# Kernel tuning notes

Hardware: AMD Instinct MI355X
Metric: run time of the kernel (lower is better)

The kernel has to match this reference:

```python
import jax, jax.numpy as jnp
import numpy as np

N, E, D, L = 50000, 640000, 128, 3  # nodes, edges, channels, layers
EPS = 1e-5


def setup_inputs() -> dict:
    key = jax.random.key(0)
    ks = jax.random.split(key, 10)
    s = 1.0 / np.sqrt(D)
    inp = {
        "x": jax.random.normal(ks[0], (N, D), dtype=jnp.float32),
        "edge_attr": jax.random.normal(ks[1], (E, D), dtype=jnp.float32),
        "w_self": jax.random.normal(ks[2], (L, D, D), dtype=jnp.float32) * s,
        "b_self": jnp.zeros((L, D), dtype=jnp.float32),
        "w_in": jax.random.normal(ks[3], (L, D, D), dtype=jnp.float32) * s,
        "b_in": jnp.zeros((L, D), dtype=jnp.float32),
        "w_rel": jax.random.normal(ks[4], (L, D, D), dtype=jnp.float32) * s,
        "b_rel": jnp.zeros((L, D), dtype=jnp.float32),
        "bn_gamma": jnp.ones((L - 1, D), dtype=jnp.float32),
        "bn_beta": jnp.zeros((L - 1, D), dtype=jnp.float32),
        "edge_index": jax.random.randint(ks[5], (2, E), 0, N, dtype=jnp.int64),
    }
    return inp


def _batchnorm(h, gamma, beta):
    mu = jnp.mean(h, axis=0)
    var = jnp.mean(jnp.square(h - mu), axis=0)  # biased var (torch BN training)
    return (h - mu) * jax.lax.rsqrt(var + EPS) * gamma + beta


def reference(x, edge_attr, w_self, b_self, w_in, b_in, w_rel, b_rel,
              bn_gamma, bn_beta, edge_index):
    src, dst = edge_index[0], edge_index[1]
    # per-node in-degree for mean aggregation (zero-degree nodes -> 0)
    cnt = jax.ops.segment_sum(jnp.ones((E, 1), x.dtype), dst, num_segments=N)
    denom = jnp.maximum(cnt, 1.0)
    for i in range(L):
        # message: lin_in(x_j * edge_attr)
        msg = jnp.einsum('ed,fd->ef', x[src] * edge_attr, w_in[i]) + b_in[i]
        agg = jax.ops.segment_sum(msg, dst, num_segments=N) / denom  # scatter-mean
        x = agg + jnp.einsum('nd,fd->nf', x, w_self[i]) + b_self[i]
        edge_attr = jnp.einsum('ed,fd->ef', edge_attr, w_rel[i]) + b_rel[i]
        if i < L - 1:
            x = jax.nn.relu(_batchnorm(x, bn_gamma[i], bn_beta[i]))
            # dropout p=0.0 -> identity
    return (x, edge_attr)
```

## Files before the change

### kernel.cpp

```cpp
#include <hip/hip_runtime.h>

#define DD 128

typedef __attribute__((ext_vector_type(8))) short bf16x8;
typedef __attribute__((ext_vector_type(4))) short bf16x4;
typedef __attribute__((ext_vector_type(4))) float f32x4;
typedef unsigned short u16;

__device__ __forceinline__ unsigned short f2bf(float f) {
  union { float f; unsigned u; } v; v.f = f;
  unsigned u = v.u;
  return (unsigned short)((u + 0x7FFFu + ((u >> 16) & 1u)) >> 16);
}
__device__ __forceinline__ float bf2f(unsigned short h) {
  union { unsigned u; float f; } v; v.u = ((unsigned)h) << 16; return v.f;
}
__device__ __forceinline__ bf16x8 pack8(f32x4 a, f32x4 b) {
  bf16x8 r;
  r[0] = (short)f2bf(a.x); r[1] = (short)f2bf(a.y);
  r[2] = (short)f2bf(a.z); r[3] = (short)f2bf(a.w);
  r[4] = (short)f2bf(b.x); r[5] = (short)f2bf(b.y);
  r[6] = (short)f2bf(b.z); r[7] = (short)f2bf(b.w);
  return r;
}

__device__ __forceinline__ bool idx_is64(const int* p) {
  return (p[1] | p[3] | p[5] | p[7]) == 0;
}
__device__ __forceinline__ int ld_idx(const int* p, long long i, bool is64) {
  return is64 ? (int)((const long long*)p)[i] : p[i];
}

__global__ void k_count(const int* __restrict__ idx, int* __restrict__ cnt, int E) {
  int e = blockIdx.x * blockDim.x + threadIdx.x;
  if (e >= E) return;
  bool is64 = idx_is64(idx);
  int d = ld_idx(idx, (long long)E + e, is64);
  atomicAdd(&cnt[d], 1);
}

__global__ __launch_bounds__(1024) void k_scan(const int* __restrict__ cnt,
    int* __restrict__ row_start, int* __restrict__ cursor, int N) {
  __shared__ int part[1024];
  int t = threadIdx.x;
  int chunk = (N + 1023) >> 10;
  int lo = t * chunk, hi = lo + chunk; if (hi > N) hi = N; if (lo > N) lo = N;
  int s = 0;
  for (int i = lo; i < hi; ++i) s += cnt[i];
  part[t] = s;
  __syncthreads();
  for (int off = 1; off < 1024; off <<= 1) {
    int v = (t >= off) ? part[t - off] : 0;
    __syncthreads();
    part[t] += v;
    __syncthreads();
  }
  int run = (t == 0) ? 0 : part[t - 1];
  for (int i = lo; i < hi; ++i) {
    row_start[i] = run; cursor[i] = run; run += cnt[i];
  }
  if (t == 1023) row_start[N] = part[1023];
}

__global__ void k_fill(const int* __restrict__ idx, int* __restrict__ cursor,
                       int* __restrict__ edge_of, int* __restrict__ src_csr,
                       int* __restrict__ inv, int E) {
  int e = blockIdx.x * blockDim.x + threadIdx.x;
  if (e >= E) return;
  bool is64 = idx_is64(idx);
  int s = ld_idx(idx, e, is64);
  int d = ld_idx(idx, (long long)E + e, is64);
  int pos = atomicAdd(&cursor[d], 1);
  edge_of[pos] = e;
  src_csr[pos] = s;
  inv[e] = pos;
}

template <int MODE>
__global__ __launch_bounds__(256) void k_layer(
    const float* __restrict__ x0, const u16* __restrict__ xbin,
    const float* __restrict__ ea0, const u16* __restrict__ eain,
    u16* __restrict__ xbout, float* __restrict__ xfout,
    u16* __restrict__ eabout, float* __restrict__ eafout,
    const int* __restrict__ row_start, const int* __restrict__ edge_of,
    const int* __restrict__ src_csr, const int* __restrict__ inv,
    const float* __restrict__ w_in, const float* __restrict__ w_self,
    const float* __restrict__ b_in, const float* __restrict__ b_self,
    const float* __restrict__ w_rel, const float* __restrict__ b_rel,
    const float* __restrict__ scale, const float* __restrict__ shift,
    float* __restrict__ gsum, float* __restrict__ gssq,
    int ntN, int ntE, int strideB) {
  __shared__ short LDS[40960];
  int bid = blockIdx.x;
  int tid = threadIdx.x;
  int wave = tid >> 6, lane = tid & 63;
  bool isA = (bid % 5) == 4;

  if (isA) {
    for (int q = tid; q < 8192; q += 256) {
      int off = q * 4;
      int f = off >> 8, k = off & 255;
      f32x4 w = (k < 128) ? *(const f32x4*)(w_in + f * 128 + k)
                          : *(const f32x4*)(w_self + f * 128 + (k - 128));
      unsigned byte = ((unsigned)(f * 512 + k * 2)) ^ (unsigned)((f & 7) << 4);
      bf16x4 s4;
      s4[0] = (short)f2bf(w.x); s4[1] = (short)f2bf(w.y);
      s4[2] = (short)f2bf(w.z); s4[3] = (short)f2bf(w.w);
      *(bf16x4*)((char*)LDS + byte) = s4;
    }
    __syncthreads();
    int tile = (bid / 5) * 4 + wave;
    if (tile >= ntN) return;
    short* aggL = LDS + 32768 + wave * 2048;
    int esub = lane >> 4, cg = lane & 15;
    int c0g = cg * 8;
    float scA[8], shA[8];
    if constexpr (MODE >= 1) {
#pragma unroll
      for (int j = 0; j < 8; ++j) { scA[j] = scale[c0g + j]; shA[j] = shift[c0g + j]; }
    }
    for (int n16 = 0; n16 < 16; ++n16) {
      int n = tile * 16 + n16;
      int s0 = row_start[n], s1 = row_start[n + 1];
      int len = s1 - s0;
      float acc[8];
#pragma unroll
      for (int j = 0; j < 8; ++j) acc[j] = 0.f;
      for (int kk = 0; kk < len; kk += 4) {
        int kx = kk + esub;
        bool act = kx < len;
        int k = s0 + (act ? kx : 0);
        if constexpr (MODE == 0) {
          int e = edge_of[k];
          int sn = src_csr[k];
          const float* ep = ea0 + (size_t)e * DD + c0g;
          f32x4 e0 = *(const f32x4*)ep, e1 = *(const f32x4*)(ep + 4);
          const float* xp = x0 + (size_t)sn * DD + c0g;
          f32x4 xv0 = *(const f32x4*)xp, xv1 = *(const f32x4*)(xp + 4);
          if (act) {
#pragma unroll
            for (int j = 0; j < 4; ++j) { acc[j] += xv0[j] * e0[j]; acc[4 + j] += xv1[j] * e1[j]; }
          }
        } else {
          int sn = src_csr[k];
          bf16x8 ev = *(const bf16x8*)(eain + (size_t)k * DD + c0g);
          bf16x8 xv = *(const bf16x8*)(xbin + (size_t)sn * DD + c0g);
          if (act) {
#pragma unroll
            for (int j = 0; j < 8; ++j) {
              float xf = fmaxf(bf2f((u16)xv[j]) * scA[j] + shA[j], 0.f);
              acc[j] += xf * bf2f((u16)ev[j]);
            }
          }
        }
      }
      float invd = (len > 0) ? 1.0f / (float)len : 0.0f;
#pragma unroll
      for (int j = 0; j < 8; ++j) {
        float s = acc[j];
        s += __shfl_xor(s, 16);
        s += __shfl_xor(s, 32);
        acc[j] = s * invd;
      }
      if (esub == 0) {
        f32x4 lo, hi;
#pragma unroll
        for (int j = 0; j < 4; ++j) { lo[j] = acc[j]; hi[j] = acc[4 + j]; }
        *(bf16x8*)(aggL + n16 * 128 + ((cg ^ (n16 & 15)) * 8)) = pack8(lo, hi);
      }
    }
    asm volatile("s_waitcnt lgkmcnt(0)" ::: "memory");
    int r = lane & 15, g = lane >> 4;
    bf16x8 a8[8];
#pragma unroll
    for (int ks = 0; ks < 4; ++ks)
      a8[ks] = *(const bf16x8*)(aggL + r * 128 + (((ks * 4 + g) ^ (r & 15)) * 8));
#pragma unroll
    for (int ks = 0; ks < 4; ++ks) {
      int c0 = ks * 32 + g * 8;
      if constexpr (MODE == 0) {
        const float* p = x0 + (size_t)(tile * 16 + r) * DD + c0;
        a8[4 + ks] = pack8(*(const f32x4*)p, *(const f32x4*)(p + 4));
      } else {
        bf16x8 raw = *(const bf16x8*)(xbin + (size_t)(tile * 16 + r) * DD + c0);
        bf16x8 fr;
#pragma unroll
        for (int j = 0; j < 8; ++j) {
          float f = fmaxf(bf2f((u16)raw[j]) * scale[c0 + j] + shift[c0 + j], 0.f);
          fr[j] = (short)f2bf(f);
        }
        a8[4 + ks] = fr;
      }
    }
    f32x4 acc4[8];
#pragma unroll
    for (int ct = 0; ct < 8; ++ct) acc4[ct] = (f32x4){0.f, 0.f, 0.f, 0.f};
#pragma unroll
    for (int ct = 0; ct < 8; ++ct) {
      int f = ct * 16 + r;
      unsigned base = (unsigned)(f * 512);
      unsigned sw = (unsigned)((f & 7) << 4);
#pragma unroll
      for (int ks = 0; ks < 8; ++ks) {
        unsigned byte = (base + (unsigned)(ks * 64 + g * 16)) ^ sw;
        bf16x8 b = *(const bf16x8*)((const char*)LDS + byte);
        acc4[ct] = __builtin_amdgcn_mfma_f32_16x16x32_bf16(a8[ks], b, acc4[ct], 0, 0, 0);
      }
    }
    int nbase = tile * 16;
    float degmask[4];
#pragma unroll
    for (int j = 0; j < 4; ++j) {
      int nn = nbase + g * 4 + j;
      degmask[j] = (row_start[nn + 1] > row_start[nn]) ? 1.0f : 0.0f;
    }
#pragma unroll
    for (int ct = 0; ct < 8; ++ct) {
      int col = ct * 16 + r;
      float bi = b_in[col], bs = b_self[col];
      float s = 0.f, s2 = 0.f;
#pragma unroll
      for (int j = 0; j < 4; ++j) {
        float v = acc4[ct][j] + bs + bi * degmask[j];
        if constexpr (MODE < 2) xbout[(size_t)(nbase + g * 4 + j) * DD + col] = f2bf(v);
        else                    xfout[(size_t)(nbase + g * 4 + j) * DD + col] = v;
        s += v; s2 += v * v;
      }
      if constexpr (MODE < 2) {
        s += __shfl_xor(s, 16);  s += __shfl_xor(s, 32);
        s2 += __shfl_xor(s2, 16); s2 += __shfl_xor(s2, 32);
        if (g == 0) { atomicAdd(&gsum[col], s); atomicAdd(&gssq[col], s2); }
      }
    }
  } else {
    int b = bid - (bid + 1) / 5;
    for (int q = tid; q < 4096; q += 256) {
      int off = q * 4;
      int f = off >> 7, d = off & 127;
      f32x4 w = *(const f32x4*)(w_rel + off);
      unsigned byte = ((unsigned)(f * 256 + d * 2)) ^ (unsigned)((f & 7) << 4);
      bf16x4 s4;
      s4[0] = (short)f2bf(w.x); s4[1] = (short)f2bf(w.y);
      s4[2] = (short)f2bf(w.z); s4[3] = (short)f2bf(w.w);
      *(bf16x4*)((char*)LDS + byte) = s4;
    }
    __syncthreads();
    int r = lane & 15, g = lane >> 4;
    for (int tile = b * 4 + wave; tile < ntE; tile += strideB) {
      bf16x8 a8[4];
      if constexpr (MODE == 0) {
        const float* rp = ea0 + (size_t)(tile * 16 + r) * DD;
#pragma unroll
        for (int ks = 0; ks < 4; ++ks) {
          const float* p = rp + ks * 32 + g * 8;
          a8[ks] = pack8(*(const f32x4*)p, *(const f32x4*)(p + 4));
        }
      } else {
        const u16* rp = eain + (size_t)(tile * 16 + r) * DD;
#pragma unroll
        for (int ks = 0; ks < 4; ++ks) a8[ks] = *(const bf16x8*)(rp + ks * 32 + g * 8);
      }
      f32x4 acc4[8];
#pragma unroll
      for (int ct = 0; ct < 8; ++ct) acc4[ct] = (f32x4){0.f, 0.f, 0.f, 0.f};
#pragma unroll
      for (int ct = 0; ct < 8; ++ct) {
        int f = ct * 16 + r;
        unsigned base = (unsigned)(f * 256);
        unsigned sw = (unsigned)((f & 7) << 4);
#pragma unroll
        for (int ks = 0; ks < 4; ++ks) {
          unsigned byte = (base + (unsigned)(ks * 64 + g * 16)) ^ sw;
          bf16x8 bb = *(const bf16x8*)((const char*)LDS + byte);
          acc4[ct] = __builtin_amdgcn_mfma_f32_16x16x32_bf16(a8[ks], bb, acc4[ct], 0, 0, 0);
        }
      }
      size_t orow[4];
#pragma unroll
      for (int j = 0; j < 4; ++j) {
        int kr = tile * 16 + g * 4 + j;
        if constexpr (MODE == 0)      orow[j] = (size_t)inv[kr];
        else if constexpr (MODE == 1) orow[j] = (size_t)kr;
        else                          orow[j] = (size_t)edge_of[kr];
      }
#pragma unroll
      for (int ct = 0; ct < 8; ++ct) {
        int col = ct * 16 + r;
        float bv = b_rel[col];
#pragma unroll
        for (int j = 0; j < 4; ++j) {
          float v = acc4[ct][j] + bv;
          if constexpr (MODE == 2) eafout[orow[j] * DD + col] = v;
          else                     eabout[orow[j] * DD + col] = f2bf(v);
        }
      }
    }
  }
}

__global__ void k_bnfin(float* __restrict__ gsum, float* __restrict__ gssq,
    const float* __restrict__ gamma, const float* __restrict__ beta,
    float* __restrict__ scale, float* __restrict__ shift, int N) {
  int d = threadIdx.x;
  float mu = gsum[d] / (float)N;
  float var = gssq[d] / (float)N - mu * mu;
  float rs = rsqrtf(var + 1e-5f);
  float sc = rs * gamma[d];
  scale[d] = sc;
  shift[d] = beta[d] - mu * sc;
  gsum[d] = 0.f;
  gssq[d] = 0.f;
}

static inline size_t alignup(size_t v, size_t a) { return (v + a - 1) & ~(a - 1); }

extern "C" void kernel_launch(void* const* d_in, const int* in_sizes, int n_in,
                              void* d_out, int out_size, void* d_ws, size_t ws_size,
                              hipStream_t stream) {
  const float* x0     = (const float*)d_in[0];
  const float* ea0    = (const float*)d_in[1];
  const float* w_self = (const float*)d_in[2];
  const float* b_self = (const float*)d_in[3];
  const float* w_in   = (const float*)d_in[4];
  const float* b_in   = (const float*)d_in[5];
  const float* w_rel  = (const float*)d_in[6];
  const float* b_rel  = (const float*)d_in[7];
  const float* gamma  = (const float*)d_in[8];
  const float* beta   = (const float*)d_in[9];
  const int*   idx    = (const int*)d_in[10];

  const int N = in_sizes[0] / DD;
  const int E = in_sizes[1] / DD;

  char* w = (char*)d_ws;
  size_t off = 0;
  int* cnt       = (int*)(w + off); off = alignup(off + (size_t)N * 4, 256);
  int* row_start = (int*)(w + off); off = alignup(off + (size_t)(N + 1) * 4, 256);
  int* cursor    = (int*)(w + off); off = alignup(off + (size_t)N * 4, 256);
  int* edge_of   = (int*)(w + off); off = alignup(off + (size_t)E * 4, 256);
  int* src_csr   = (int*)(w + off); off = alignup(off + (size_t)E * 4, 256);
  int* inv       = (int*)(w + off); off = alignup(off + (size_t)E * 4, 256);
  float* gstats  = (float*)(w + off); off = alignup(off + 256 * 4, 256);
  float* scale   = (float*)(w + off); off = alignup(off + 128 * 4, 256);
  float* shift   = (float*)(w + off); off = alignup(off + 128 * 4, 256);
  u16* xbA       = (u16*)(w + off); off = alignup(off + (size_t)N * DD * 2, 256);
  u16* xbB       = (u16*)(w + off); off = alignup(off + (size_t)N * DD * 2, 256);
  u16* eaA       = (u16*)(w + off); off = alignup(off + (size_t)E * DD * 2, 256);
  u16* eaB       = (u16*)(w + off); off = alignup(off + (size_t)E * DD * 2, 256);
  float* gsum = gstats, *gssq = gstats + 128;
  (void)ws_size; (void)n_in; (void)out_size;

  float* out_x  = (float*)d_out;
  float* out_ea = out_x + (size_t)N * DD;

  (void)hipMemsetAsync(cnt, 0, (size_t)N * 4, stream);
  int ethreads = 256, eblocks = (E + ethreads - 1) / ethreads;
  k_count<<<eblocks, ethreads, 0, stream>>>(idx, cnt, E);
  k_scan<<<1, 1024, 0, stream>>>(cnt, row_start, cursor, N);
  k_fill<<<eblocks, ethreads, 0, stream>>>(idx, cursor, edge_of, src_csr, inv, E);
  (void)hipMemsetAsync(gstats, 0, 256 * 4, stream);

  const int ntN = N / 16;
  const int ntE = E / 16;
  const int nA = (ntN + 3) / 4;
  const int grid = nA * 5;
  const int strideB = (grid - nA) * 4;

  k_layer<0><<<grid, 256, 0, stream>>>(x0, nullptr, ea0, nullptr,
      xbA, nullptr, eaA, nullptr,
      row_start, edge_of, src_csr, inv,
      w_in, w_self, b_in, b_self, w_rel, b_rel,
      scale, shift, gsum, gssq, ntN, ntE, strideB);
  k_bnfin<<<1, 128, 0, stream>>>(gsum, gssq, gamma, beta, scale, shift, N);

  k_layer<1><<<grid, 256, 0, stream>>>(nullptr, xbA, nullptr, eaA,
      xbB, nullptr, eaB, nullptr,
      row_start, edge_of, src_csr, inv,
      w_in + DD * DD, w_self + DD * DD, b_in + DD, b_self + DD,
      w_rel + DD * DD, b_rel + DD,
      scale, shift, gsum, gssq, ntN, ntE, strideB);
  k_bnfin<<<1, 128, 0, stream>>>(gsum, gssq, gamma + DD, beta + DD, scale, shift, N);

  k_layer<2><<<grid, 256, 0, stream>>>(nullptr, xbB, nullptr, eaB,
      nullptr, out_x, nullptr, out_ea,
      row_start, edge_of, src_csr, inv,
      w_in + 2 * DD * DD, w_self + 2 * DD * DD, b_in + 2 * DD, b_self + 2 * DD,
      w_rel + 2 * DD * DD, b_rel + 2 * DD,
      scale, shift, gsum, gssq, ntN, ntE, strideB);
}
```

Before: 1.103 ms.

## Split fused layer kernel into per-node aggregation/edge-GEMM and separate node GEMM

Result: faster. 1.029 ms (-6.8%).

```diff
diff --git a/kernel.cpp b/kernel.cpp
--- a/kernel.cpp
+++ b/kernel.cpp
@@ -63,8 +63,7 @@
 }
 
 __global__ void k_fill(const int* __restrict__ idx, int* __restrict__ cursor,
-                       int* __restrict__ edge_of, int* __restrict__ src_csr,
-                       int* __restrict__ inv, int E) {
+                       int* __restrict__ edge_of, int* __restrict__ src_csr, int E) {
   int e = blockIdx.x * blockDim.x + threadIdx.x;
   if (e >= E) return;
   bool is64 = idx_is64(idx);
@@ -73,167 +72,100 @@
   int pos = atomicAdd(&cursor[d], 1);
   edge_of[pos] = e;
   src_csr[pos] = s;
-  inv[e] = pos;
 }
 
 template <int MODE>
-__global__ __launch_bounds__(256) void k_layer(
+__global__ __launch_bounds__(256, 4) void k_ar(
     const float* __restrict__ x0, const u16* __restrict__ xbin,
     const float* __restrict__ ea0, const u16* __restrict__ eain,
-    u16* __restrict__ xbout, float* __restrict__ xfout,
     u16* __restrict__ eabout, float* __restrict__ eafout,
+    float* __restrict__ aggmf, u16* __restrict__ aggm,
     const int* __restrict__ row_start, const int* __restrict__ edge_of,
-    const int* __restrict__ src_csr, const int* __restrict__ inv,
-    const float* __restrict__ w_in, const float* __restrict__ w_self,
-    const float* __restrict__ b_in, const float* __restrict__ b_self,
+    const int* __restrict__ src_csr,
     const float* __restrict__ w_rel, const float* __restrict__ b_rel,
     const float* __restrict__ scale, const float* __restrict__ shift,
-    float* __restrict__ gsum, float* __restrict__ gssq,
-    int ntN, int ntE, int strideB) {
-  __shared__ short LDS[40960];
+    int nA, int ntE) {
+  __shared__ short Wl[16384];
   int bid = blockIdx.x;
   int tid = threadIdx.x;
   int wave = tid >> 6, lane = tid & 63;
-  bool isA = (bid % 5) == 4;
-
-  if (isA) {
-    for (int q = tid; q < 8192; q += 256) {
-      int off = q * 4;
-      int f = off >> 8, k = off & 255;
-      f32x4 w = (k < 128) ? *(const f32x4*)(w_in + f * 128 + k)
-                          : *(const f32x4*)(w_self + f * 128 + (k - 128));
-      unsigned byte = ((unsigned)(f * 512 + k * 2)) ^ (unsigned)((f & 7) << 4);
-      bf16x4 s4;
-      s4[0] = (short)f2bf(w.x); s4[1] = (short)f2bf(w.y);
-      s4[2] = (short)f2bf(w.z); s4[3] = (short)f2bf(w.w);
-      *(bf16x4*)((char*)LDS + byte) = s4;
-    }
-    __syncthreads();
-    int tile = (bid / 5) * 4 + wave;
-    if (tile >= ntN) return;
-    short* aggL = LDS + 32768 + wave * 2048;
+  (void)aggmf;
+
+  if (bid < nA) {
+    int n = bid * 4 + wave;
     int esub = lane >> 4, cg = lane & 15;
-    int c0g = cg * 8;
+    int c0 = cg * 8;
     float scA[8], shA[8];
     if constexpr (MODE >= 1) {
 #pragma unroll
-      for (int j = 0; j < 8; ++j) { scA[j] = scale[c0g + j]; shA[j] = shift[c0g + j]; }
-    }
-    for (int n16 = 0; n16 < 16; ++n16) {
-      int n = tile * 16 + n16;
-      int s0 = row_start[n], s1 = row_start[n + 1];
-      int len = s1 - s0;
-      float acc[8];
-#pragma unroll
-      for (int j = 0; j < 8; ++j) acc[j] = 0.f;
-      for (int kk = 0; kk < len; kk += 4) {
-        int kx = kk + esub;
-        bool act = kx < len;
-        int k = s0 + (act ? kx : 0);
-        if constexpr (MODE == 0) {
-          int e = edge_of[k];
-          int sn = src_csr[k];
-          const float* ep = ea0 + (size_t)e * DD + c0g;
-          f32x4 e0 = *(const f32x4*)ep, e1 = *(const f32x4*)(ep + 4);
-          const float* xp = x0 + (size_t)sn * DD + c0g;
-          f32x4 xv0 = *(const f32x4*)xp, xv1 = *(const f32x4*)(xp + 4);
-          if (act) {
-#pragma unroll
-            for (int j = 0; j < 4; ++j) { acc[j] += xv0[j] * e0[j]; acc[4 + j] += xv1[j] * e1[j]; }
+      for (int j = 0; j < 8; ++j) { scA[j] = scale[c0 + j]; shA[j] = shift[c0 + j]; }
+    }
+    int s0 = row_start[n], s1 = row_start[n + 1];
+    int len = s1 - s0;
+    float acc[8];
+#pragma unroll
+    for (int j = 0; j < 8; ++j) acc[j] = 0.f;
+    for (int kk = 0; kk < len; kk += 8) {
+      int kx0 = kk + esub, kx1 = kk + 4 + esub;
+      bool a0 = kx0 < len, a1 = kx1 < len;
+      int k0 = s0 + (a0 ? kx0 : 0);
+      int k1 = s0 + (a1 ? kx1 : 0);
+      if constexpr (MODE == 0) {
+        int e0 = edge_of[k0], e1 = edge_of[k1];
+        int sn0 = src_csr[k0], sn1 = src_csr[k1];
+        const float* ep0 = ea0 + (size_t)e0 * DD + c0;
+        const float* ep1 = ea0 + (size_t)e1 * DD + c0;
+        const float* xp0 = x0 + (size_t)sn0 * DD + c0;
+        const float* xp1 = x0 + (size_t)sn1 * DD + c0;
+        f32x4 ea0a = *(const f32x4*)ep0, ea0b = *(const f32x4*)(ep0 + 4);
+        f32x4 ea1a = *(const f32x4*)ep1, ea1b = *(const f32x4*)(ep1 + 4);
+        f32x4 xv0a = *(const f32x4*)xp0, xv0b = *(const f32x4*)(xp0 + 4);
+        f32x4 xv1a = *(const f32x4*)xp1, xv1b = *(const f32x4*)(xp1 + 4);
+        if (a0) {
+#pragma unroll
+          for (int j = 0; j < 4; ++j) { acc[j] += xv0a[j] * ea0a[j]; acc[4 + j] += xv0b[j] * ea0b[j]; }
+        }
+        if (a1) {
+#pragma unroll
+          for (int j = 0; j < 4; ++j) { acc[j] += xv1a[j] * ea1a[j]; acc[4 + j] += xv1b[j] * ea1b[j]; }
+        }
+      } else {
+        int sn0 = src_csr[k0], sn1 = src_csr[k1];
+        bf16x8 ev0 = *(const bf16x8*)(eain + (size_t)k0 * DD + c0);
+        bf16x8 ev1 = *(const bf16x8*)(eain + (size_t)k1 * DD + c0);
+        bf16x8 xv0 = *(const bf16x8*)(xbin + (size_t)sn0 * DD + c0);
+        bf16x8 xv1 = *(const bf16x8*)(xbin + (size_t)sn1 * DD + c0);
+        if (a0) {
+#pragma unroll
+          for (int j = 0; j < 8; ++j) {
+            float xf = fmaxf(bf2f((u16)xv0[j]) * scA[j] + shA[j], 0.f);
+            acc[j] += xf * bf2f((u16)ev0[j]);
           }
-        } else {
-          int sn = src_csr[k];
-          bf16x8 ev = *(const bf16x8*)(eain + (size_t)k * DD + c0g);
-          bf16x8 xv = *(const bf16x8*)(xbin + (size_t)sn * DD + c0g);
-          if (act) {
-#pragma unroll
-            for (int j = 0; j < 8; ++j) {
-              float xf = fmaxf(bf2f((u16)xv[j]) * scA[j] + shA[j], 0.f);
-              acc[j] += xf * bf2f((u16)ev[j]);
-            }
+        }
+        if (a1) {
+#pragma unroll
+          for (int j = 0; j < 8; ++j) {
+            float xf = fmaxf(bf2f((u16)xv1[j]) * scA[j] + shA[j], 0.f);
+            acc[j] += xf * bf2f((u16)ev1[j]);
           }
         }
       }
-      float invd = (len > 0) ? 1.0f / (float)len : 0.0f;
-#pragma unroll
-      for (int j = 0; j < 8; ++j) {
-        float s = acc[j];
-        s += __shfl_xor(s, 16);
-        s += __shfl_xor(s, 32);
-        acc[j] = s * invd;
-      }
-      if (esub == 0) {
-        f32x4 lo, hi;
-#pragma unroll
-        for (int j = 0; j < 4; ++j) { lo[j] = acc[j]; hi[j] = acc[4 + j]; }
-        *(bf16x8*)(aggL + n16 * 128 + ((cg ^ (n16 & 15)) * 8)) = pack8(lo, hi);
-      }
-    }
-    asm volatile("s_waitcnt lgkmcnt(0)" ::: "memory");
-    int r = lane & 15, g = lane >> 4;
-    bf16x8 a8[8];
-#pragma unroll
-    for (int ks = 0; ks < 4; ++ks)
-      a8[ks] = *(const bf16x8*)(aggL + r * 128 + (((ks * 4 + g) ^ (r & 15)) * 8));
-#pragma unroll
-    for (int ks = 0; ks < 4; ++ks) {
-      int c0 = ks * 32 + g * 8;
-      if constexpr (MODE == 0) {
-        const float* p = x0 + (size_t)(tile * 16 + r) * DD + c0;
-        a8[4 + ks] = pack8(*(const f32x4*)p, *(const f32x4*)(p + 4));
-      } else {
-        bf16x8 raw = *(const bf16x8*)(xbin + (size_t)(tile * 16 + r) * DD + c0);
-        bf16x8 fr;
-#pragma unroll
-        for (int j = 0; j < 8; ++j) {
-          float f = fmaxf(bf2f((u16)raw[j]) * scale[c0 + j] + shift[c0 + j], 0.f);
-          fr[j] = (short)f2bf(f);
-        }
-        a8[4 + ks] = fr;
-      }
-    }
-    f32x4 acc4[8];
-#pragma unroll
-    for (int ct = 0; ct < 8; ++ct) acc4[ct] = (f32x4){0.f, 0.f, 0.f, 0.f};
-#pragma unroll
-    for (int ct = 0; ct < 8; ++ct) {
-      int f = ct * 16 + r;
-      unsigned base = (unsigned)(f * 512);
-      unsigned sw = (unsigned)((f & 7) << 4);
-#pragma unroll
-      for (int ks = 0; ks < 8; ++ks) {
-        unsigned byte = (base + (unsigned)(ks * 64 + g * 16)) ^ sw;
-        bf16x8 b = *(const bf16x8*)((const char*)LDS + byte);
-        acc4[ct] = __builtin_amdgcn_mfma_f32_16x16x32_bf16(a8[ks], b, acc4[ct], 0, 0, 0);
-      }
-    }
-    int nbase = tile * 16;
-    float degmask[4];
-#pragma unroll
-    for (int j = 0; j < 4; ++j) {
-      int nn = nbase + g * 4 + j;
-      degmask[j] = (row_start[nn + 1] > row_start[nn]) ? 1.0f : 0.0f;
-    }
-#pragma unroll
-    for (int ct = 0; ct < 8; ++ct) {
-      int col = ct * 16 + r;
-      float bi = b_in[col], bs = b_self[col];
-      float s = 0.f, s2 = 0.f;
-#pragma unroll
-      for (int j = 0; j < 4; ++j) {
-        float v = acc4[ct][j] + bs + bi * degmask[j];
-        if constexpr (MODE < 2) xbout[(size_t)(nbase + g * 4 + j) * DD + col] = f2bf(v);
-        else                    xfout[(size_t)(nbase + g * 4 + j) * DD + col] = v;
-        s += v; s2 += v * v;
-      }
-      if constexpr (MODE < 2) {
-        s += __shfl_xor(s, 16);  s += __shfl_xor(s, 32);
-        s2 += __shfl_xor(s2, 16); s2 += __shfl_xor(s2, 32);
-        if (g == 0) { atomicAdd(&gsum[col], s); atomicAdd(&gssq[col], s2); }
-      }
+    }
+    float invd = (len > 0) ? 1.0f / (float)len : 0.0f;
+#pragma unroll
+    for (int j = 0; j < 8; ++j) {
+      float s = acc[j];
+      s += __shfl_xor(s, 16);
+      s += __shfl_xor(s, 32);
+      acc[j] = s * invd;
+    }
+    if (esub == 0) {
+      f32x4 lo, hi;
+#pragma unroll
+      for (int j = 0; j < 4; ++j) { lo[j] = acc[j]; hi[j] = acc[4 + j]; }
+      *(bf16x8*)(aggm + (size_t)n * DD + c0) = pack8(lo, hi);
     }
   } else {
-    int b = bid - (bid + 1) / 5;
     for (int q = tid; q < 4096; q += 256) {
       int off = q * 4;
       int f = off >> 7, d = off & 127;
@@ -242,58 +174,149 @@
       bf16x4 s4;
       s4[0] = (short)f2bf(w.x); s4[1] = (short)f2bf(w.y);
       s4[2] = (short)f2bf(w.z); s4[3] = (short)f2bf(w.w);
-      *(bf16x4*)((char*)LDS + byte) = s4;
+      *(bf16x4*)((char*)Wl + byte) = s4;
     }
     __syncthreads();
     int r = lane & 15, g = lane >> 4;
-    for (int tile = b * 4 + wave; tile < ntE; tile += strideB) {
-      bf16x8 a8[4];
-      if constexpr (MODE == 0) {
-        const float* rp = ea0 + (size_t)(tile * 16 + r) * DD;
-#pragma unroll
-        for (int ks = 0; ks < 4; ++ks) {
-          const float* p = rp + ks * 32 + g * 8;
-          a8[ks] = pack8(*(const f32x4*)p, *(const f32x4*)(p + 4));
-        }
-      } else {
-        const u16* rp = eain + (size_t)(tile * 16 + r) * DD;
-#pragma unroll
-        for (int ks = 0; ks < 4; ++ks) a8[ks] = *(const bf16x8*)(rp + ks * 32 + g * 8);
+    int tile = (bid - nA) * 4 + wave;
+    if (tile >= ntE) return;
+    bf16x8 a8[4];
+    if constexpr (MODE == 0) {
+      int er = edge_of[tile * 16 + r];
+      const float* rp = ea0 + (size_t)er * DD;
+#pragma unroll
+      for (int ks = 0; ks < 4; ++ks) {
+        const float* p = rp + ks * 32 + g * 8;
+        a8[ks] = pack8(*(const f32x4*)p, *(const f32x4*)(p + 4));
       }
-      f32x4 acc4[8];
-#pragma unroll
-      for (int ct = 0; ct < 8; ++ct) acc4[ct] = (f32x4){0.f, 0.f, 0.f, 0.f};
-#pragma unroll
-      for (int ct = 0; ct < 8; ++ct) {
-        int f = ct * 16 + r;
-        unsigned base = (unsigned)(f * 256);
-        unsigned sw = (unsigned)((f & 7) << 4);
-#pragma unroll
-        for (int ks = 0; ks < 4; ++ks) {
-          unsigned byte = (base + (unsigned)(ks * 64 + g * 16)) ^ sw;
-          bf16x8 bb = *(const bf16x8*)((const char*)LDS + byte);
-          acc4[ct] = __builtin_amdgcn_mfma_f32_16x16x32_bf16(a8[ks], bb, acc4[ct], 0, 0, 0);
-        }
+    } else {
+      const u16* rp = eain + (size_t)(tile * 16 + r) * DD;
+#pragma unroll
+      for (int ks = 0; ks < 4; ++ks) a8[ks] = *(const bf16x8*)(rp + ks * 32 + g * 8);
+    }
+    f32x4 acc4[8];
+#pragma unroll
+    for (int ct = 0; ct < 8; ++ct) acc4[ct] = (f32x4){0.f, 0.f, 0.f, 0.f};
+#pragma unroll
+    for (int ct = 0; ct < 8; ++ct) {
+      int f = ct * 16 + r;
+      unsigned base = (unsigned)(f * 256);
+      unsigned sw = (unsigned)((f & 7) << 4);
+#pragma unroll
+      for (int ks = 0; ks < 4; ++ks) {
+        unsigned byte = (base + (unsigned)(ks * 64 + g * 16)) ^ sw;
+        bf16x8 bb = *(const bf16x8*)((const char*)Wl + byte);
+        acc4[ct] = __builtin_amdgcn_mfma_f32_16x16x32_bf16(a8[ks], bb, acc4[ct], 0, 0, 0);
       }
-      size_t orow[4];
+    }
+    size_t orow[4];
+#pragma unroll
+    for (int j = 0; j < 4; ++j) {
+      int kr = tile * 16 + g * 4 + j;
+      if constexpr (MODE == 2) orow[j] = (size_t)edge_of[kr];
+      else                     orow[j] = (size_t)kr;
+    }
+#pragma unroll
+    for (int ct = 0; ct < 8; ++ct) {
+      int col = ct * 16 + r;
+      float bv = b_rel[col];
 #pragma unroll
       for (int j = 0; j < 4; ++j) {
-        int kr = tile * 16 + g * 4 + j;
-        if constexpr (MODE == 0)      orow[j] = (size_t)inv[kr];
-        else if constexpr (MODE == 1) orow[j] = (size_t)kr;
-        else                          orow[j] = (size_t)edge_of[kr];
+        float v = acc4[ct][j] + bv;
+        if constexpr (MODE == 2) eafout[orow[j] * DD + col] = v;
+        else                     eabout[orow[j] * DD + col] = f2bf(v);
       }
-#pragma unroll
-      for (int ct = 0; ct < 8; ++ct) {
-        int col = ct * 16 + r;
-        float bv = b_rel[col];
-#pragma unroll
-        for (int j = 0; j < 4; ++j) {
-          float v = acc4[ct][j] + bv;
-          if constexpr (MODE == 2) eafout[orow[j] * DD + col] = v;
-          else                     eabout[orow[j] * DD + col] = f2bf(v);
-        }
+    }
+  }
+}
+
+template <typename TX, bool BN, typename TO, bool STATS>
+__global__ __launch_bounds__(256, 2) void k_node(const u16* __restrict__ aggm,
+    const TX* __restrict__ xc, const float* __restrict__ W_in,
+    const float* __restrict__ W_self, const float* __restrict__ b_in,
+    const float* __restrict__ b_self, const int* __restrict__ row_start,
+    const float* __restrict__ scale, const float* __restrict__ shift,
+    TO* __restrict__ xn, float* __restrict__ gsum, float* __restrict__ gssq,
+    int ntiles) {
+  __shared__ short Wl[DD * 256];
+  for (int q = threadIdx.x; q < DD * 256 / 4; q += 256) {
+    int off = q * 4;
+    int f = off >> 8, k = off & 255;
+    f32x4 w = (k < 128) ? *(const f32x4*)(W_in + f * 128 + k)
+                        : *(const f32x4*)(W_self + f * 128 + (k - 128));
+    unsigned byte = ((unsigned)(f * 512 + k * 2)) ^ (unsigned)((f & 7) << 4);
+    bf16x4 s4;
+    s4[0] = (short)f2bf(w.x); s4[1] = (short)f2bf(w.y);
+    s4[2] = (short)f2bf(w.z); s4[3] = (short)f2bf(w.w);
+    *(bf16x4*)((char*)Wl + byte) = s4;
+  }
+  __syncthreads();
+  int wave = threadIdx.x >> 6, lane = threadIdx.x & 63;
+  int tile = blockIdx.x * 4 + wave;
+  if (tile >= ntiles) return;
+  int r = lane & 15, g = lane >> 4;
+  int arowi = tile * 16 + r;
+  const u16* arow = aggm + (size_t)arowi * DD;
+  const TX* xrow = xc + (size_t)arowi * DD;
+  bf16x8 a[8];
+#pragma unroll
+  for (int ks = 0; ks < 4; ++ks) a[ks] = *(const bf16x8*)(arow + ks * 32 + g * 8);
+#pragma unroll
+  for (int ks = 0; ks < 4; ++ks) {
+    int c0 = ks * 32 + g * 8;
+    if constexpr (sizeof(TX) == 2) {
+      bf16x8 raw = *(const bf16x8*)(xrow + c0);
+      bf16x8 fr;
+#pragma unroll
+      for (int j = 0; j < 8; ++j) {
+        float f = bf2f((u16)raw[j]);
+        if constexpr (BN) f = fmaxf(f * scale[c0 + j] + shift[c0 + j], 0.f);
+        fr[j] = (short)f2bf(f);
       }
+      a[4 + ks] = fr;
+    } else {
+      const float* p = (const float*)xrow + c0;
+      a[4 + ks] = pack8(*(const f32x4*)p, *(const f32x4*)(p + 4));
+    }
+  }
+  f32x4 acc[8];
+#pragma unroll
+  for (int ct = 0; ct < 8; ++ct) acc[ct] = (f32x4){0.f, 0.f, 0.f, 0.f};
+#pragma unroll
+  for (int ct = 0; ct < 8; ++ct) {
+    int f = ct * 16 + r;
+    unsigned base = (unsigned)(f * 512);
+    unsigned sw = (unsigned)((f & 7) << 4);
+#pragma unroll
+    for (int ks = 0; ks < 8; ++ks) {
+      unsigned byte = (base + (unsigned)(ks * 64 + g * 16)) ^ sw;
+      bf16x8 b = *(const bf16x8*)((const char*)Wl + byte);
+      acc[ct] = __builtin_amdgcn_mfma_f32_16x16x32_bf16(a[ks], b, acc[ct], 0, 0, 0);
+    }
+  }
+  int nbase = tile * 16;
+  float degmask[4];
+#pragma unroll
+  for (int j = 0; j < 4; ++j) {
+    int nn = nbase + g * 4 + j;
+    degmask[j] = (row_start[nn + 1] > row_start[nn]) ? 1.0f : 0.0f;
+  }
+#pragma unroll
+  for (int ct = 0; ct < 8; ++ct) {
+    int col = ct * 16 + r;
+    float bi = b_in[col], bs = b_self[col];
+    float s = 0.f, s2 = 0.f;
+#pragma unroll
+    for (int j = 0; j < 4; ++j) {
+      float v = acc[ct][j] + bs + bi * degmask[j];
+      if constexpr (sizeof(TO) == 2) xn[(size_t)(nbase + g * 4 + j) * DD + col] = (TO)f2bf(v);
+      else                            xn[(size_t)(nbase + g * 4 + j) * DD + col] = (TO)v;
+      s += v; s2 += v * v;
+    }
+    if constexpr (STATS) {
+      s += __shfl_xor(s, 16);  s += __shfl_xor(s, 32);
+      s2 += __shfl_xor(s2, 16); s2 += __shfl_xor(s2, 32);
+      if (g == 0) { atomicAdd(&gsum[col], s); atomicAdd(&gssq[col], s2); }
     }
   }
 }
@@ -339,10 +362,10 @@
   int* cursor    = (int*)(w + off); off = alignup(off + (size_t)N * 4, 256);
   int* edge_of   = (int*)(w + off); off = alignup(off + (size_t)E * 4, 256);
   int* src_csr   = (int*)(w + off); off = alignup(off + (size_t)E * 4, 256);
-  int* inv       = (int*)(w + off); off = alignup(off + (size_t)E * 4, 256);
   float* gstats  = (float*)(w + off); off = alignup(off + 256 * 4, 256);
   float* scale   = (float*)(w + off); off = alignup(off + 128 * 4, 256);
   float* shift   = (float*)(w + off); off = alignup(off + 128 * 4, 256);
+  u16* aggm      = (u16*)(w + off); off = alignup(off + (size_t)N * DD * 2, 256);
   u16* xbA       = (u16*)(w + off); off = alignup(off + (size_t)N * DD * 2, 256);
   u16* xbB       = (u16*)(w + off); off = alignup(off + (size_t)N * DD * 2, 256);
   u16* eaA       = (u16*)(w + off); off = alignup(off + (size_t)E * DD * 2, 256);
@@ -357,34 +380,36 @@
   int ethreads = 256, eblocks = (E + ethreads - 1) / ethreads;
   k_count<<<eblocks, ethreads, 0, stream>>>(idx, cnt, E);
   k_scan<<<1, 1024, 0, stream>>>(cnt, row_start, cursor, N);
-  k_fill<<<eblocks, ethreads, 0, stream>>>(idx, cursor, edge_of, src_csr, inv, E);
+  k_fill<<<eblocks, ethreads, 0, stream>>>(idx, cursor, edge_of, src_csr, E);
   (void)hipMemsetAsync(gstats, 0, 256 * 4, stream);
 
   const int ntN = N / 16;
   const int ntE = E / 16;
-  const int nA = (ntN + 3) / 4;
-  const int grid = nA * 5;
-  const int strideB = (grid - nA) * 4;
-
-  k_layer<0><<<grid, 256, 0, stream>>>(x0, nullptr, ea0, nullptr,
-      xbA, nullptr, eaA, nullptr,
-      row_start, edge_of, src_csr, inv,
-      w_in, w_self, b_in, b_self, w_rel, b_rel,
-      scale, shift, gsum, gssq, ntN, ntE, strideB);
+  const int nA = (N + 3) / 4;
+  const int nB = (ntE + 3) / 4;
+  const int grid = nA + nB;
+  const int nodeBlocks = (ntN + 3) / 4;
+
+  k_ar<0><<<grid, 256, 0, stream>>>(x0, nullptr, ea0, nullptr,
+      eaA, nullptr, nullptr, aggm, row_start, edge_of, src_csr,
+      w_rel, b_rel, scale, shift, nA, ntE);
+  k_node<float, false, u16, true><<<nodeBlocks, 256, 0, stream>>>(aggm, x0,
+      w_in, w_self, b_in, b_self, row_start, scale, shift,
+      xbA, gsum, gssq, ntN);
   k_bnfin<<<1, 128, 0, stream>>>(gsum, gssq, gamma, beta, scale, shift, N);
 
-  k_layer<1><<<grid, 256, 0, stream>>>(nullptr, xbA, nullptr, eaA,
-      xbB, nullptr, eaB, nullptr,
-      row_start, edge_of, src_csr, inv,
+  k_ar<1><<<grid, 256, 0, stream>>>(nullptr, xbA, nullptr, eaA,
+      eaB, nullptr, nullptr, aggm, row_start, edge_of, src_csr,
+      w_rel + DD * DD, b_rel + DD, scale, shift, nA, ntE);
+  k_node<u16, true, u16, true><<<nodeBlocks, 256, 0, stream>>>(aggm, xbA,
       w_in + DD * DD, w_self + DD * DD, b_in + DD, b_self + DD,
-      w_rel + DD * DD, b_rel + DD,
-      scale, shift, gsum, gssq, ntN, ntE, strideB);
+      row_start, scale, shift, xbB, gsum, gssq, ntN);
   k_bnfin<<<1, 128, 0, stream>>>(gsum, gssq, gamma + DD, beta + DD, scale, shift, N);
 
-  k_layer<2><<<grid, 256, 0, stream>>>(nullptr, xbB, nullptr, eaB,
-      nullptr, out_x, nullptr, out_ea,
-      row_start, edge_of, src_csr, inv,
+  k_ar<2><<<grid, 256, 0, stream>>>(nullptr, xbB, nullptr, eaB,
+      nullptr, out_ea, nullptr, aggm, row_start, edge_of, src_csr,
+      w_rel + 2 * DD * DD, b_rel + 2 * DD, scale, shift, nA, ntE);
+  k_node<u16, true, float, false><<<nodeBlocks, 256, 0, stream>>>(aggm, xbB,
       w_in + 2 * DD * DD, w_self + 2 * DD * DD, b_in + 2 * DD, b_self + 2 * DD,
-      w_rel + 2 * DD * DD, b_rel + 2 * DD,
-      scale, shift, gsum, gssq, ntN, ntE, strideB);
-}
+      row_start, scale, shift, out_x, gsum, gssq, ntN);
+}
```
